# Performance work log

Measured on AMD Instinct MI355X. Metric: run time of the kernel, lower is better.

## Reference

```python
import jax, jax.numpy as jnp
import numpy as np

N = 100_000      # nodes
E = 1_600_000    # edges (avg degree 16)
D = 64           # node feature dim
C = 2            # num_classes
K = 2            # propagation hops


def setup_inputs() -> dict:
    key = jax.random.key(0)
    k1, k2, k3 = jax.random.split(key, 3)
    x = jax.random.normal(k1, (N, D), dtype=jnp.float32)
    edge_index = jax.random.randint(k2, (2, E), 0, N, dtype=jnp.int64)
    W = jax.random.normal(k3, (C, D), dtype=jnp.float32) * 0.1  # torch Linear weight [out,in]
    b = jnp.zeros((C,), dtype=jnp.float32)
    return {"x": x, "edge_index": edge_index, "W": W, "b": b}


def reference(x, edge_index, W, b):
    n = x.shape[0]
    self_loop = jnp.arange(n, dtype=edge_index.dtype)
    row = jnp.concatenate([edge_index[0], self_loop])  # source
    col = jnp.concatenate([edge_index[1], self_loop])  # target
    # GCN symmetric normalization with self-loops (PyG gcn_norm)
    deg = jax.ops.segment_sum(jnp.ones(col.shape, dtype=x.dtype), col, num_segments=n)
    dinv = jnp.where(deg > 0, jax.lax.rsqrt(deg), 0.0)
    norm = dinv[row] * dinv[col]                      # [E+N]
    # K-hop propagation: x <- A_hat x
    for _ in range(K):
        x = jax.ops.segment_sum(norm[:, None] * x[row], col, num_segments=n)
    logits = x @ W.T + b                               # [N, C]
    return jax.nn.log_softmax(logits, axis=1)
```

## Files before the change

kernel.cpp:

```cpp
#include <hip/hip_runtime.h>
#include <hip/hip_bf16.h>
#include <math.h>


#define NODES 100000
#define EDGES 1600000
#define DIM 64

#define PBITS 12
#define PSIZE 4096
#define P_BUCKETS 25
#define CAP 160000
#define NSLICE 10
#define PART_BLOCKS 256
#define SEG (EDGES / PART_BLOCKS)

__global__ void detect_init_kernel(const void* ei, int* mode, int* cursor) {
  int t = threadIdx.x;
  const int* p = (const int*)ei;
  unsigned long long ball = __ballot(p[2 * t + 1] == 0);
  if (t == 0) *mode = (ball == ~0ULL) ? 1 : 0;
  if (t < P_BUCKETS) cursor[t] = t * CAP;
}

__global__ void partition_kernel(const void* ei, const int* __restrict__ mode,
                                 int* __restrict__ cursor,
                                 int* __restrict__ rbuf,
                                 int* __restrict__ cbuf) {
  __shared__ int lcnt[P_BUCKETS];
  __shared__ int lbase[P_BUCKETS];
  int t = threadIdx.x;
  int m = *mode;
  int beg = blockIdx.x * SEG;
  int end = beg + SEG;

  if (t < P_BUCKETS) lcnt[t] = 0;
  __syncthreads();

  for (int e = beg + t; e < end; e += 256) {
    int c = m ? (int)((const long long*)ei)[EDGES + e]
              : ((const int*)ei)[EDGES + e];
    atomicAdd(&lcnt[c >> PBITS], 1);
  }
  __syncthreads();
  if (t < P_BUCKETS) {
    lbase[t] = atomicAdd(&cursor[t], lcnt[t]);
    lcnt[t] = 0;
  }
  __syncthreads();

  for (int e = beg + t; e < end; e += 256) {
    int r, c;
    if (m) {
      r = (int)((const long long*)ei)[e];
      c = (int)((const long long*)ei)[EDGES + e];
    } else {
      r = ((const int*)ei)[e];
      c = ((const int*)ei)[EDGES + e];
    }
    int b = c >> PBITS;
    int pos = lbase[b] + atomicAdd(&lcnt[b], 1);
    if (pos < (b + 1) * CAP) {
      rbuf[pos] = r;
      cbuf[pos] = c;
    }
  }
}

__global__ void deg_kernel(const int* __restrict__ cursor,
                           const int* __restrict__ cbuf,
                           int* __restrict__ dpart) {
  __shared__ int lds[PSIZE];
  int p = blockIdx.x / NSLICE, s = blockIdx.x % NSLICE;
  for (int i = threadIdx.x; i < PSIZE; i += 256) lds[i] = 0;
  __syncthreads();
  int base = p * CAP;
  int cnt = min(cursor[p] - base, CAP);
  int per = (cnt + NSLICE - 1) / NSLICE;
  int beg = base + s * per;
  int end = min(base + cnt, beg + per);
  for (int e = beg + threadIdx.x; e < end; e += 256)
    atomicAdd(&lds[cbuf[e] & (PSIZE - 1)], 1);
  __syncthreads();
  int* out = dpart + (size_t)blockIdx.x * PSIZE;
  for (int i = threadIdx.x; i < PSIZE; i += 256) out[i] = lds[i];
}

__global__ void dinv_merge_kernel(const int* __restrict__ dpart,
                                  float* __restrict__ dinv) {
  int i = blockIdx.x * blockDim.x + threadIdx.x;
  if (i >= NODES) return;
  int p = i >> PBITS, l = i & (PSIZE - 1);
  int d = 0;
#pragma unroll
  for (int s = 0; s < NSLICE; s++) d += dpart[(size_t)(p * NSLICE + s) * PSIZE + l];
  dinv[i] = rsqrtf((float)(d + 1));
}

__global__ void proj_kernel(const float* __restrict__ x,
                            const float* __restrict__ W,
                            const float* __restrict__ dinv,
                            float2* __restrict__ ts) {
  int wid = (blockIdx.x * (blockDim.x >> 6)) + (threadIdx.x >> 6);
  int d = threadIdx.x & 63;
  if (wid >= NODES) return;
  float xv = x[(size_t)wid * DIM + d];
  float p0 = xv * W[d];
  float p1 = xv * W[DIM + d];
#pragma unroll
  for (int off = 32; off >= 1; off >>= 1) {
    p0 += __shfl_xor(p0, off, 64);
    p1 += __shfl_xor(p1, off, 64);
  }
  if (d == 0) {
    float di = dinv[wid];
    float2 t;
    t.x = di * p0;
    t.y = di * p1;
    ts[wid] = t;
  }
}

__global__ void hop_kernel(const int* __restrict__ cursor,
                           const int* __restrict__ rbuf,
                           const int* __restrict__ cbuf,
                           const float2* __restrict__ feat,
                           float2* __restrict__ hpart) {
  __shared__ float lx[PSIZE];
  __shared__ float ly[PSIZE];
  int p = blockIdx.x / NSLICE, s = blockIdx.x % NSLICE;
  for (int i = threadIdx.x; i < PSIZE; i += 256) {
    lx[i] = 0.f;
    ly[i] = 0.f;
  }
  __syncthreads();
  int base = p * CAP;
  int cnt = min(cursor[p] - base, CAP);
  int per = (cnt + NSLICE - 1) / NSLICE;
  int beg = base + s * per;
  int end = min(base + cnt, beg + per);
  for (int e = beg + threadIdx.x; e < end; e += 256) {
    int r = rbuf[e];
    int cl = cbuf[e] & (PSIZE - 1);
    float2 v = feat[r];
    atomicAdd(&lx[cl], v.x);
    atomicAdd(&ly[cl], v.y);
  }
  __syncthreads();
  float2* out = hpart + (size_t)blockIdx.x * PSIZE;
  for (int i = threadIdx.x; i < PSIZE; i += 256) {
    float2 o;
    o.x = lx[i];
    o.y = ly[i];
    out[i] = o;
  }
}

__global__ void merge1_kernel(const float2* __restrict__ hpart,
                              const float2* __restrict__ ts,
                              const float* __restrict__ dinv,
                              float2* __restrict__ z) {
  int i = blockIdx.x * blockDim.x + threadIdx.x;
  if (i >= NODES) return;
  int p = i >> PBITS, l = i & (PSIZE - 1);
  float2 t0 = ts[i];
  float ax = t0.x, ay = t0.y;
#pragma unroll
  for (int s = 0; s < NSLICE; s++) {
    float2 v = hpart[(size_t)(p * NSLICE + s) * PSIZE + l];
    ax += v.x;
    ay += v.y;
  }
  float di = dinv[i];
  float sc = di * di;
  float2 o;
  o.x = sc * ax;
  o.y = sc * ay;
  z[i] = o;
}

__global__ void merge2_kernel(const float2* __restrict__ hpart,
                              const float2* __restrict__ z,
                              const float* __restrict__ dinv,
                              const float* __restrict__ bias,
                              float2* __restrict__ out) {
  int i = blockIdx.x * blockDim.x + threadIdx.x;
  if (i >= NODES) return;
  int p = i >> PBITS, l = i & (PSIZE - 1);
  float2 z0 = z[i];
  float ax = z0.x, ay = z0.y;
#pragma unroll
  for (int s = 0; s < NSLICE; s++) {
    float2 v = hpart[(size_t)(p * NSLICE + s) * PSIZE + l];
    ax += v.x;
    ay += v.y;
  }
  float di = dinv[i];
  float l0 = di * ax + bias[0];
  float l1 = di * ay + bias[1];
  float m = fmaxf(l0, l1);
  float ls = m + logf(expf(l0 - m) + expf(l1 - m));
  float2 o;
  o.x = l0 - ls;
  o.y = l1 - ls;
  out[i] = o;
}

extern "C" void kernel_launch(void* const* d_in, const int* in_sizes, int n_in,
                              void* d_out, int out_size, void* d_ws,
                              size_t ws_size, hipStream_t stream) {
  const float* x = (const float*)d_in[0];
  const void* ei = d_in[1];
  const float* W = (const float*)d_in[2];
  const float* b = (const float*)d_in[3];
  float2* out = (float2*)d_out;

  char* w = (char*)d_ws;
  size_t off = 0;
  auto alloc = [&](size_t bytes) -> char* {
    char* p = w + off;
    off += (bytes + 255) & ~(size_t)255;
    return p;
  };
  int* mode = (int*)alloc(sizeof(int));
  int* cursor = (int*)alloc(P_BUCKETS * sizeof(int));
  int* rbuf = (int*)alloc((size_t)P_BUCKETS * CAP * sizeof(int));
  int* cbuf = (int*)alloc((size_t)P_BUCKETS * CAP * sizeof(int));
  int* dpart = (int*)alloc((size_t)P_BUCKETS * NSLICE * PSIZE * sizeof(int));
  float* dinv = (float*)alloc(NODES * sizeof(float));
  float2* ts = (float2*)alloc(NODES * sizeof(float2));
  float2* z = (float2*)alloc(NODES * sizeof(float2));
  float2* hpart =
      (float2*)alloc((size_t)P_BUCKETS * NSLICE * PSIZE * sizeof(float2));
  (void)ws_size;

  const int NGRID = (NODES + 255) / 256;

  detect_init_kernel<<<1, 64, 0, stream>>>(ei, mode, cursor);
  partition_kernel<<<PART_BLOCKS, 256, 0, stream>>>(ei, mode, cursor, rbuf,
                                                    cbuf);
  deg_kernel<<<P_BUCKETS * NSLICE, 256, 0, stream>>>(cursor, cbuf, dpart);
  dinv_merge_kernel<<<NGRID, 256, 0, stream>>>(dpart, dinv);

  const int WPB = 256 / 64;
  proj_kernel<<<(NODES + WPB - 1) / WPB, 256, 0, stream>>>(x, W, dinv, ts);

  hop_kernel<<<P_BUCKETS * NSLICE, 256, 0, stream>>>(cursor, rbuf, cbuf, ts,
                                                     hpart);
  merge1_kernel<<<NGRID, 256, 0, stream>>>(hpart, ts, dinv, z);
  hop_kernel<<<P_BUCKETS * NSLICE, 256, 0, stream>>>(cursor, rbuf, cbuf, z,
                                                     hpart);
  merge2_kernel<<<NGRID, 256, 0, stream>>>(hpart, z, dinv, b, out);
}
```

Before: 178.4 us.

## Interleave edge buffers, vectorize partition loads, fuse degree with dinv

The partition step now reads edge indices two at a time with vector loads. It writes each edge as one int2 holding the source and the local target, replacing separate row and column buffers. The degree pass runs one 1024-thread block per bucket and writes dinv directly, which drops the per-slice partial histograms and the separate merge kernel. The hop kernel moves to 512-thread blocks and loads the packed edge once per iteration. The bucket capacity shrinks to 131072, which risks dropping edges if a bucket overflows, though uniform random targets average about 65k per bucket.

```diff
diff --git a/kernel.cpp b/kernel.cpp
--- a/kernel.cpp
+++ b/kernel.cpp
@@ -10,12 +10,13 @@
 #define PBITS 12
 #define PSIZE 4096
 #define P_BUCKETS 25
-#define CAP 160000
+#define CAP 131072
 #define NSLICE 10
 #define PART_BLOCKS 256
 #define SEG (EDGES / PART_BLOCKS)
-
-__global__ void detect_init_kernel(const void* ei, int* mode, int* cursor) {
+#define PAIRS (SEG / 2)
+
+__global__ void init_kernel(const void* ei, int* mode, int* cursor) {
   int t = threadIdx.x;
   const int* p = (const int*)ei;
   unsigned long long ball = __ballot(p[2 * t + 1] == 0);
@@ -25,22 +26,31 @@
 
 __global__ void partition_kernel(const void* ei, const int* __restrict__ mode,
                                  int* __restrict__ cursor,
-                                 int* __restrict__ rbuf,
-                                 int* __restrict__ cbuf) {
+                                 int2* __restrict__ ecbuf) {
   __shared__ int lcnt[P_BUCKETS];
   __shared__ int lbase[P_BUCKETS];
   int t = threadIdx.x;
   int m = *mode;
-  int beg = blockIdx.x * SEG;
-  int end = beg + SEG;
+  int pbase = blockIdx.x * PAIRS;
 
   if (t < P_BUCKETS) lcnt[t] = 0;
   __syncthreads();
 
-  for (int e = beg + t; e < end; e += 256) {
-    int c = m ? (int)((const long long*)ei)[EDGES + e]
-              : ((const int*)ei)[EDGES + e];
-    atomicAdd(&lcnt[c >> PBITS], 1);
+  if (m) {
+    const longlong2* cp =
+        (const longlong2*)((const long long*)ei + EDGES) + pbase;
+    for (int i = t; i < PAIRS; i += 256) {
+      longlong2 v = cp[i];
+      atomicAdd(&lcnt[((int)v.x) >> PBITS], 1);
+      atomicAdd(&lcnt[((int)v.y) >> PBITS], 1);
+    }
+  } else {
+    const int2* cp = (const int2*)((const int*)ei + EDGES) + pbase;
+    for (int i = t; i < PAIRS; i += 256) {
+      int2 v = cp[i];
+      atomicAdd(&lcnt[v.x >> PBITS], 1);
+      atomicAdd(&lcnt[v.y >> PBITS], 1);
+    }
   }
   __syncthreads();
   if (t < P_BUCKETS) {
@@ -49,52 +59,55 @@
   }
   __syncthreads();
 
-  for (int e = beg + t; e < end; e += 256) {
-    int r, c;
-    if (m) {
-      r = (int)((const long long*)ei)[e];
-      c = (int)((const long long*)ei)[EDGES + e];
-    } else {
-      r = ((const int*)ei)[e];
-      c = ((const int*)ei)[EDGES + e];
-    }
-    int b = c >> PBITS;
-    int pos = lbase[b] + atomicAdd(&lcnt[b], 1);
-    if (pos < (b + 1) * CAP) {
-      rbuf[pos] = r;
-      cbuf[pos] = c;
+  if (m) {
+    const longlong2* rp = (const longlong2*)ei + pbase;
+    const longlong2* cp =
+        (const longlong2*)((const long long*)ei + EDGES) + pbase;
+    for (int i = t; i < PAIRS; i += 256) {
+      longlong2 rv = rp[i];
+      longlong2 cv = cp[i];
+      int r0 = (int)rv.x, c0 = (int)cv.x;
+      int b0 = c0 >> PBITS;
+      int p0 = lbase[b0] + atomicAdd(&lcnt[b0], 1);
+      if (p0 < (b0 + 1) * CAP) ecbuf[p0] = make_int2(r0, c0 & (PSIZE - 1));
+      int r1 = (int)rv.y, c1 = (int)cv.y;
+      int b1 = c1 >> PBITS;
+      int p1 = lbase[b1] + atomicAdd(&lcnt[b1], 1);
+      if (p1 < (b1 + 1) * CAP) ecbuf[p1] = make_int2(r1, c1 & (PSIZE - 1));
+    }
+  } else {
+    const int2* rp = (const int2*)ei + pbase;
+    const int2* cp = (const int2*)((const int*)ei + EDGES) + pbase;
+    for (int i = t; i < PAIRS; i += 256) {
+      int2 rv = rp[i];
+      int2 cv = cp[i];
+      int b0 = cv.x >> PBITS;
+      int p0 = lbase[b0] + atomicAdd(&lcnt[b0], 1);
+      if (p0 < (b0 + 1) * CAP) ecbuf[p0] = make_int2(rv.x, cv.x & (PSIZE - 1));
+      int b1 = cv.y >> PBITS;
+      int p1 = lbase[b1] + atomicAdd(&lcnt[b1], 1);
+      if (p1 < (b1 + 1) * CAP) ecbuf[p1] = make_int2(rv.y, cv.y & (PSIZE - 1));
     }
   }
 }
 
 __global__ void deg_kernel(const int* __restrict__ cursor,
-                           const int* __restrict__ cbuf,
-                           int* __restrict__ dpart) {
-  __shared__ int lds[PSIZE];
-  int p = blockIdx.x / NSLICE, s = blockIdx.x % NSLICE;
-  for (int i = threadIdx.x; i < PSIZE; i += 256) lds[i] = 0;
+                           const int2* __restrict__ ecbuf,
+                           float* __restrict__ dinv) {
+  __shared__ int h[PSIZE];
+  int p = blockIdx.x;
+  for (int i = threadIdx.x; i < PSIZE; i += 1024) h[i] = 0;
   __syncthreads();
   int base = p * CAP;
   int cnt = min(cursor[p] - base, CAP);
-  int per = (cnt + NSLICE - 1) / NSLICE;
-  int beg = base + s * per;
-  int end = min(base + cnt, beg + per);
-  for (int e = beg + threadIdx.x; e < end; e += 256)
-    atomicAdd(&lds[cbuf[e] & (PSIZE - 1)], 1);
-  __syncthreads();
-  int* out = dpart + (size_t)blockIdx.x * PSIZE;
-  for (int i = threadIdx.x; i < PSIZE; i += 256) out[i] = lds[i];
-}
-
-__global__ void dinv_merge_kernel(const int* __restrict__ dpart,
-                                  float* __restrict__ dinv) {
-  int i = blockIdx.x * blockDim.x + threadIdx.x;
-  if (i >= NODES) return;
-  int p = i >> PBITS, l = i & (PSIZE - 1);
-  int d = 0;
-#pragma unroll
-  for (int s = 0; s < NSLICE; s++) d += dpart[(size_t)(p * NSLICE + s) * PSIZE + l];
-  dinv[i] = rsqrtf((float)(d + 1));
+  for (int e = threadIdx.x; e < cnt; e += 1024)
+    atomicAdd(&h[ecbuf[base + e].y], 1);
+  __syncthreads();
+  int gbase = p << PBITS;
+  for (int i = threadIdx.x; i < PSIZE; i += 1024) {
+    int g = gbase + i;
+    if (g < NODES) dinv[g] = rsqrtf((float)(h[i] + 1));
+  }
 }
 
 __global__ void proj_kernel(const float* __restrict__ x,
@@ -122,14 +135,13 @@
 }
 
 __global__ void hop_kernel(const int* __restrict__ cursor,
-                           const int* __restrict__ rbuf,
-                           const int* __restrict__ cbuf,
+                           const int2* __restrict__ ecbuf,
                            const float2* __restrict__ feat,
                            float2* __restrict__ hpart) {
   __shared__ float lx[PSIZE];
   __shared__ float ly[PSIZE];
   int p = blockIdx.x / NSLICE, s = blockIdx.x % NSLICE;
-  for (int i = threadIdx.x; i < PSIZE; i += 256) {
+  for (int i = threadIdx.x; i < PSIZE; i += 512) {
     lx[i] = 0.f;
     ly[i] = 0.f;
   }
@@ -139,20 +151,19 @@
   int per = (cnt + NSLICE - 1) / NSLICE;
   int beg = base + s * per;
   int end = min(base + cnt, beg + per);
-  for (int e = beg + threadIdx.x; e < end; e += 256) {
-    int r = rbuf[e];
-    int cl = cbuf[e] & (PSIZE - 1);
-    float2 v = feat[r];
-    atomicAdd(&lx[cl], v.x);
-    atomicAdd(&ly[cl], v.y);
-  }
-  __syncthreads();
-  float2* out = hpart + (size_t)blockIdx.x * PSIZE;
-  for (int i = threadIdx.x; i < PSIZE; i += 256) {
+  for (int e = beg + threadIdx.x; e < end; e += 512) {
+    int2 ec = ecbuf[e];
+    float2 v = feat[ec.x];
+    atomicAdd(&lx[ec.y], v.x);
+    atomicAdd(&ly[ec.y], v.y);
+  }
+  __syncthreads();
+  float2* outp = hpart + (size_t)blockIdx.x * PSIZE;
+  for (int i = threadIdx.x; i < PSIZE; i += 512) {
     float2 o;
     o.x = lx[i];
     o.y = ly[i];
-    out[i] = o;
+    outp[i] = o;
   }
 }
 
@@ -224,9 +235,7 @@
   };
   int* mode = (int*)alloc(sizeof(int));
   int* cursor = (int*)alloc(P_BUCKETS * sizeof(int));
-  int* rbuf = (int*)alloc((size_t)P_BUCKETS * CAP * sizeof(int));
-  int* cbuf = (int*)alloc((size_t)P_BUCKETS * CAP * sizeof(int));
-  int* dpart = (int*)alloc((size_t)P_BUCKETS * NSLICE * PSIZE * sizeof(int));
+  int2* ecbuf = (int2*)alloc((size_t)P_BUCKETS * CAP * sizeof(int2));
   float* dinv = (float*)alloc(NODES * sizeof(float));
   float2* ts = (float2*)alloc(NODES * sizeof(float2));
   float2* z = (float2*)alloc(NODES * sizeof(float2));
@@ -236,19 +245,15 @@
 
   const int NGRID = (NODES + 255) / 256;
 
-  detect_init_kernel<<<1, 64, 0, stream>>>(ei, mode, cursor);
-  partition_kernel<<<PART_BLOCKS, 256, 0, stream>>>(ei, mode, cursor, rbuf,
-                                                    cbuf);
-  deg_kernel<<<P_BUCKETS * NSLICE, 256, 0, stream>>>(cursor, cbuf, dpart);
-  dinv_merge_kernel<<<NGRID, 256, 0, stream>>>(dpart, dinv);
+  init_kernel<<<1, 64, 0, stream>>>(ei, mode, cursor);
+  partition_kernel<<<PART_BLOCKS, 256, 0, stream>>>(ei, mode, cursor, ecbuf);
+  deg_kernel<<<P_BUCKETS, 1024, 0, stream>>>(cursor, ecbuf, dinv);
 
   const int WPB = 256 / 64;
   proj_kernel<<<(NODES + WPB - 1) / WPB, 256, 0, stream>>>(x, W, dinv, ts);
 
-  hop_kernel<<<P_BUCKETS * NSLICE, 256, 0, stream>>>(cursor, rbuf, cbuf, ts,
-                                                     hpart);
+  hop_kernel<<<P_BUCKETS * NSLICE, 512, 0, stream>>>(cursor, ecbuf, ts, hpart);
   merge1_kernel<<<NGRID, 256, 0, stream>>>(hpart, ts, dinv, z);
-  hop_kernel<<<P_BUCKETS * NSLICE, 256, 0, stream>>>(cursor, rbuf, cbuf, z,
-                                                     hpart);
+  hop_kernel<<<P_BUCKETS * NSLICE, 512, 0, stream>>>(cursor, ecbuf, z, hpart);
   merge2_kernel<<<NGRID, 256, 0, stream>>>(hpart, z, dinv, b, out);
 }
```

Measured after the change: 177.4 us. No clear change (-0.6%).
